# Kernel optimization log

Measured on AMD Instinct MI355X. Metric: run time of the kernel, lower is better.

Reference implementation:

```python
import jax, jax.numpy as jnp
import numpy as np

EMBED = 1024
HEADS = 16
HEAD_DIM = EMBED // HEADS


def setup_inputs() -> dict:
    key = jax.random.key(0)
    ks = jax.random.split(key, 7)
    B, Sd, Se = 4, 2048, 2048
    dec = jax.random.normal(ks[0], (B, Sd, EMBED), dtype=jnp.float32)
    enc = jax.random.normal(ks[1], (B, Se, EMBED), dtype=jnp.float32)
    scale = 1.0 / np.sqrt(EMBED)
    W_q = jax.random.normal(ks[2], (EMBED, EMBED), dtype=jnp.float32) * scale
    W_k = jax.random.normal(ks[3], (EMBED, EMBED), dtype=jnp.float32) * scale
    W_v = jax.random.normal(ks[4], (EMBED, EMBED), dtype=jnp.float32) * scale
    W_o = jax.random.normal(ks[5], (EMBED, EMBED), dtype=jnp.float32) * scale
    b_o = jax.random.normal(ks[6], (EMBED,), dtype=jnp.float32) * 0.01
    return {"decoder_input": dec, "encoder_output": enc,
            "W_q": W_q, "W_k": W_k, "W_v": W_v, "W_o": W_o, "b_o": b_o}


def reference(decoder_input, encoder_output, W_q, W_k, W_v, W_o, b_o):
    B, Sd, E = decoder_input.shape
    Se = encoder_output.shape[1]
    # projections (nn.Linear applies x @ W.T; here W is stored as [in, out])
    Q = (decoder_input @ W_q).reshape(B, Sd, HEADS, HEAD_DIM)
    K = (encoder_output @ W_k).reshape(B, Se, HEADS, HEAD_DIM)
    V = (encoder_output @ W_v).reshape(B, Se, HEADS, HEAD_DIM)
    # scores: [B, H, Sd, Se]
    scores = jnp.einsum('bqhd,bkhd->bhqk', Q, K) / jnp.sqrt(jnp.float32(HEAD_DIM))
    attn = jax.nn.softmax(scores, axis=-1)
    out = jnp.einsum('bhqk,bkhd->bqhd', attn, V).reshape(B, Sd, E)
    return out @ W_o + b_o
```

## Files before the change

kernel.cpp:

```cpp
#include <hip/hip_runtime.h>
#include <hip/hip_bf16.h>

namespace {

typedef __attribute__((ext_vector_type(8))) short bf16x8;
typedef __attribute__((ext_vector_type(4))) float f32x4;
typedef __attribute__((ext_vector_type(4))) unsigned u32x4v;

constexpr int BATCH = 4;
constexpr int SEQ   = 2048;
constexpr int EMB   = 1024;
constexpr int NH    = 16;
constexpr int HD    = 64;
constexpr int MTOT  = BATCH * SEQ;
constexpr int KVW   = 2 * EMB;
constexpr float LOG2E = 1.44269504088896f;
constexpr float SOFTMAX_C = 16.0f;

__device__ __forceinline__ unsigned short f2bf(float x) {
    unsigned int u = __float_as_uint(x);
    u += 0x7fffu + ((u >> 16) & 1u);
    return (unsigned short)(u >> 16);
}

__device__ __forceinline__ void gl_lds16(const void* g, void* l) {
    __builtin_amdgcn_global_load_lds(
        (const __attribute__((address_space(1))) unsigned int*)g,
        (__attribute__((address_space(3))) unsigned int*)l, 16, 0, 0);
}

__global__ __launch_bounds__(256)
void conv_bf16(const float* __restrict__ dec, const float* __restrict__ enc,
               unsigned short* __restrict__ decb, unsigned short* __restrict__ encb,
               int n4)
{
    int i = blockIdx.x * 256 + threadIdx.x;
    if (i >= n4) return;
    const float* src = blockIdx.y ? enc : dec;
    unsigned short* dst = blockIdx.y ? encb : decb;
    float4 v = ((const float4*)src)[i];
    ushort4 o;
    o.x = f2bf(v.x); o.y = f2bf(v.y); o.z = f2bf(v.z); o.w = f2bf(v.w);
    ((ushort4*)dst)[i] = o;
}

__global__ __launch_bounds__(256)
void wtrans(const float* __restrict__ W0, const float* __restrict__ W1,
            const float* __restrict__ W2, const float* __restrict__ W3,
            unsigned short* __restrict__ WtBase, float qscale)
{
    __shared__ __align__(16) unsigned short Ts[64][65];
    const int tid = threadIdx.x;
    const int z = blockIdx.z;
    const float* W = (z == 0) ? W0 : (z == 1) ? W1 : (z == 2) ? W2 : W3;
    unsigned short* Wt = WtBase + (size_t)z * EMB * EMB;
    const float scale = (z == 0) ? qscale : 1.0f;
    const int n0 = blockIdx.x * 64, k0 = blockIdx.y * 64;
    #pragma unroll
    for (int i = 0; i < 4; ++i) {
        int id = tid + i * 256;
        int r = id >> 4, q = id & 15;
        float4 v = *(const float4*)&W[(size_t)(k0 + r) * EMB + n0 + q * 4];
        Ts[q * 4 + 0][r] = f2bf(v.x * scale);
        Ts[q * 4 + 1][r] = f2bf(v.y * scale);
        Ts[q * 4 + 2][r] = f2bf(v.z * scale);
        Ts[q * 4 + 3][r] = f2bf(v.w * scale);
    }
    __syncthreads();
    #pragma unroll
    for (int i = 0; i < 4; ++i) {
        int id = tid + i * 256;
        int rn = id >> 4, q = id & 15;
        ushort4 o;
        o.x = Ts[rn][q * 4 + 0]; o.y = Ts[rn][q * 4 + 1];
        o.z = Ts[rn][q * 4 + 2]; o.w = Ts[rn][q * 4 + 3];
        *(ushort4*)&Wt[(size_t)(n0 + rn) * EMB + k0 + q * 4] = o;
    }
}

__global__ __launch_bounds__(256)
void vtrans(const unsigned short* __restrict__ V, unsigned short* __restrict__ Vt)
{
    __shared__ __align__(16) unsigned short Ts[64][72];
    const int tid = threadIdx.x;
    const int s0 = blockIdx.x * 64;
    const int bh = blockIdx.y, b = bh >> 4, h = bh & 15;
    #pragma unroll
    for (int it = 0; it < 2; ++it) {
        int id = tid + it * 256;
        int r = id >> 3, seg = id & 7;
        uint4 v = *(const uint4*)&V[(size_t)(b * SEQ + s0 + r) * KVW + h * HD + seg * 8];
        const unsigned short* pv = (const unsigned short*)&v;
        #pragma unroll
        for (int j = 0; j < 8; ++j) Ts[seg * 8 + j][r] = pv[j];
    }
    __syncthreads();
    #pragma unroll
    for (int it = 0; it < 2; ++it) {
        int id = tid + it * 256;
        int d = id >> 3, sg = id & 7;
        int base = (sg >> 2) * 32 + (sg & 3) * 4;
        uint2 wlo = *(const uint2*)&Ts[d][base];
        uint2 whi = *(const uint2*)&Ts[d][base + 16];
        uint4 w;
        w.x = wlo.x; w.y = wlo.y; w.z = whi.x; w.w = whi.y;
        *(uint4*)&Vt[((size_t)bh * HD + d) * SEQ + s0 + sg * 8] = w;
    }
}

template<bool OUT_BF16, bool BIAS>
__device__ __forceinline__
void gemm_body(const unsigned short* __restrict__ A, const unsigned short* __restrict__ Bt,
               const float* __restrict__ bias, void* __restrict__ Cout,
               int m0, int n0, int N, int Kd)
{
    __shared__ __align__(16) unsigned short As[2][128 * 32];
    __shared__ __align__(16) unsigned short Bs[2][128 * 32];
    const int tid  = threadIdx.x;
    const int lane = tid & 63, wave = tid >> 6;
    const int g = lane >> 4, c = lane & 15;
    const int wm = (wave & 1) * 64, wn = (wave >> 1) * 64;

    const int r0 = tid >> 2, s = tid & 3;
    const int sg = s ^ ((r0 + (r0 >> 2)) & 3);
    const unsigned short* ga0 = A  + (size_t)(m0 + r0)      * Kd + sg * 8;
    const unsigned short* ga1 = A  + (size_t)(m0 + r0 + 64) * Kd + sg * 8;
    const unsigned short* gb0 = Bt + (size_t)(n0 + r0)      * Kd + sg * 8;
    const unsigned short* gb1 = Bt + (size_t)(n0 + r0 + 64) * Kd + sg * 8;
    const int lo0 = tid * 8, lo1 = (256 + tid) * 8;

    const int cs = (c + (c >> 2)) & 3;

    f32x4 acc[4][4];
    #pragma unroll
    for (int i = 0; i < 4; ++i)
        #pragma unroll
        for (int j = 0; j < 4; ++j) acc[i][j] = (f32x4)0.0f;

    gl_lds16(ga0, &As[0][lo0]); gl_lds16(ga1, &As[0][lo1]);
    gl_lds16(gb0, &Bs[0][lo0]); gl_lds16(gb1, &Bs[0][lo1]);
    ga0 += 32; ga1 += 32; gb0 += 32; gb1 += 32;
    __syncthreads();

    const int KT = Kd / 32;
    for (int kt = 0; kt < KT; kt += 2) {
        #pragma unroll
        for (int h2 = 0; h2 < 2; ++h2) {
            const int k = kt + h2;
            if (k + 1 < KT) {
                gl_lds16(ga0, &As[h2 ^ 1][lo0]); gl_lds16(ga1, &As[h2 ^ 1][lo1]);
                gl_lds16(gb0, &Bs[h2 ^ 1][lo0]); gl_lds16(gb1, &Bs[h2 ^ 1][lo1]);
                ga0 += 32; ga1 += 32; gb0 += 32; gb1 += 32;
            }
            bf16x8 af[4], bfr[4];
            #pragma unroll
            for (int mt = 0; mt < 4; ++mt)
                af[mt]  = *(const bf16x8*)&As[h2][(wm + mt * 16 + c) * 32 + (g ^ cs) * 8];
            #pragma unroll
            for (int nt = 0; nt < 4; ++nt)
                bfr[nt] = *(const bf16x8*)&Bs[h2][(wn + nt * 16 + c) * 32 + (g ^ cs) * 8];
            #pragma unroll
            for (int mt = 0; mt < 4; ++mt)
                #pragma unroll
                for (int nt = 0; nt < 4; ++nt)
                    acc[mt][nt] = __builtin_amdgcn_mfma_f32_16x16x32_bf16(af[mt], bfr[nt], acc[mt][nt], 0, 0, 0);
            __syncthreads();
        }
    }

    #pragma unroll
    for (int mt = 0; mt < 4; ++mt) {
        #pragma unroll
        for (int nt = 0; nt < 4; ++nt) {
            int n = n0 + wn + nt * 16 + c;
            float bv = BIAS ? bias[n] : 0.0f;
            #pragma unroll
            for (int r = 0; r < 4; ++r) {
                int m = m0 + wm + mt * 16 + 4 * g + r;
                float v = acc[mt][nt][r] + bv;
                if (OUT_BF16) ((unsigned short*)Cout)[(size_t)m * N + n] = f2bf(v);
                else          ((float*)Cout)[(size_t)m * N + n] = v;
            }
        }
    }
}

__global__ __launch_bounds__(256)
void proj_fused(const unsigned short* __restrict__ decb, const unsigned short* __restrict__ encb,
                const unsigned short* __restrict__ WtBase,
                unsigned short* __restrict__ Qb, unsigned short* __restrict__ KVb)
{
    const int fid = blockIdx.y * 24 + blockIdx.x;
    const int xcd = fid & 7, idx = fid >> 3;
    const int mt  = (xcd << 3) | (idx / 24);
    const int nt  = idx % 24;
    const int m0  = mt * 128;
    if (nt < 8) {
        gemm_body<true, false>(decb, WtBase, nullptr, Qb, m0, nt * 128, EMB, EMB);
    } else {
        gemm_body<true, false>(encb, WtBase + (size_t)EMB * EMB, nullptr, KVb,
                               m0, (nt - 8) * 128, KVW, EMB);
    }
}

__global__ __launch_bounds__(256)
void proj_out(const unsigned short* __restrict__ Ob, const unsigned short* __restrict__ WoT,
              const float* __restrict__ bo, float* __restrict__ out)
{
    const int fid = blockIdx.y * 8 + blockIdx.x;
    const int xcd = fid & 7, idx = fid >> 3;
    const int mt  = (xcd << 3) | (idx >> 3);
    const int nt  = idx & 7;
    gemm_body<false, true>(Ob, WoT, bo, out, mt * 128, nt * 128, EMB, EMB);
}

__global__ __launch_bounds__(256)
void attn(const unsigned short* __restrict__ Q, const unsigned short* __restrict__ KV,
          const unsigned short* __restrict__ Vt, unsigned short* __restrict__ O)
{
    __shared__ __align__(16) unsigned short Ks[2][64 * 64];
    __shared__ __align__(16) unsigned short Vs[2][64 * 64];

    const int tid  = threadIdx.x;
    const int lane = tid & 63, wave = tid >> 6;
    const int g = lane >> 4, c = lane & 15, c7 = c & 7;

    const int fid  = blockIdx.y * 32 + blockIdx.x;
    const int xcd  = fid & 7, idx = fid >> 3;
    const int bh   = (xcd << 3) | (idx >> 5);
    const int qblk = idx & 31;
    const int b = bh >> 4, h = bh & 15;
    const int qw = qblk * 64 + wave * 16;

    const unsigned short* Qp0 = Q + (size_t)(b * SEQ + qw + c) * EMB + h * HD;
    bf16x8 qb[2];
    qb[0] = *(const bf16x8*)(Qp0 + g * 8);
    qb[1] = *(const bf16x8*)(Qp0 + 32 + g * 8);

    const int r0 = tid >> 3, s8 = tid & 7;
    const int sg = s8 ^ (r0 & 7);
    const unsigned short* gK0 = KV + ((size_t)b * SEQ + r0) * KVW + h * HD + sg * 8;
    const unsigned short* gK1 = gK0 + (size_t)32 * KVW;
    const unsigned short* gV0 = Vt + (size_t)bh * HD * SEQ + (size_t)r0 * SEQ + sg * 8;
    const unsigned short* gV1 = gV0 + (size_t)32 * SEQ;
    const int lo0 = tid * 8, lo1 = (256 + tid) * 8;

    f32x4 oac[4];
    #pragma unroll
    for (int dt = 0; dt < 4; ++dt) oac[dt] = (f32x4)0.0f;
    f32x4 lacc = (f32x4)0.0f;
    const f32x4 minit = {-SOFTMAX_C, -SOFTMAX_C, -SOFTMAX_C, -SOFTMAX_C};
    const short onebf = (short)0x3F80;
    const bf16x8 vones = {onebf, onebf, onebf, onebf, onebf, onebf, onebf, onebf};

    gl_lds16(gK0, &Ks[0][lo0]); gl_lds16(gK1, &Ks[0][lo1]);
    gl_lds16(gV0, &Vs[0][lo0]); gl_lds16(gV1, &Vs[0][lo1]);
    gK0 += (size_t)64 * KVW; gK1 += (size_t)64 * KVW; gV0 += 64; gV1 += 64;
    __syncthreads();

    constexpr int T = SEQ / 64;
    for (int t = 0; t < T; t += 2) {
        #pragma unroll
        for (int h2 = 0; h2 < 2; ++h2) {
            const int tt = t + h2;
            if (tt + 1 < T) {
                gl_lds16(gK0, &Ks[h2 ^ 1][lo0]); gl_lds16(gK1, &Ks[h2 ^ 1][lo1]);
                gl_lds16(gV0, &Vs[h2 ^ 1][lo0]); gl_lds16(gV1, &Vs[h2 ^ 1][lo1]);
                gK0 += (size_t)64 * KVW; gK1 += (size_t)64 * KVW;
                gV0 += 64;               gV1 += 64;
            }

            f32x4 st[4];
            __builtin_amdgcn_s_setprio(1);
            #pragma unroll
            for (int kt = 0; kt < 4; ++kt) {
                bf16x8 ka0 = *(const bf16x8*)&Ks[h2][(kt * 16 + c) * 64 + (g ^ c7) * 8];
                bf16x8 ka1 = *(const bf16x8*)&Ks[h2][(kt * 16 + c) * 64 + ((4 + g) ^ c7) * 8];
                st[kt] = __builtin_amdgcn_mfma_f32_16x16x32_bf16(ka0, qb[0], minit, 0, 0, 0);
                st[kt] = __builtin_amdgcn_mfma_f32_16x16x32_bf16(ka1, qb[1], st[kt], 0, 0, 0);
            }
            __builtin_amdgcn_s_setprio(0);

            bf16x8 pa[2];
            {
                unsigned uu[8];
                #pragma unroll
                for (int kt = 0; kt < 4; ++kt) {
                    float p0 = __builtin_amdgcn_exp2f(st[kt][0]);
                    float p1 = __builtin_amdgcn_exp2f(st[kt][1]);
                    float p2 = __builtin_amdgcn_exp2f(st[kt][2]);
                    float p3 = __builtin_amdgcn_exp2f(st[kt][3]);
                    asm("v_cvt_pk_bf16_f32 %0, %1, %2" : "=v"(uu[2 * kt])     : "v"(p0), "v"(p1));
                    asm("v_cvt_pk_bf16_f32 %0, %1, %2" : "=v"(uu[2 * kt + 1]) : "v"(p2), "v"(p3));
                }
                u32x4v w0 = {uu[0], uu[1], uu[2], uu[3]};
                u32x4v w1 = {uu[4], uu[5], uu[6], uu[7]};
                pa[0] = __builtin_bit_cast(bf16x8, w0);
                pa[1] = __builtin_bit_cast(bf16x8, w1);
            }

            __builtin_amdgcn_s_setprio(1);
            #pragma unroll
            for (int dt = 0; dt < 4; ++dt) {
                bf16x8 vb0 = *(const bf16x8*)&Vs[h2][(dt * 16 + c) * 64 + (g ^ c7) * 8];
                bf16x8 vb1 = *(const bf16x8*)&Vs[h2][(dt * 16 + c) * 64 + ((4 + g) ^ c7) * 8];
                oac[dt] = __builtin_amdgcn_mfma_f32_16x16x32_bf16(pa[0], vb0, oac[dt], 0, 0, 0);
                oac[dt] = __builtin_amdgcn_mfma_f32_16x16x32_bf16(pa[1], vb1, oac[dt], 0, 0, 0);
            }
            lacc = __builtin_amdgcn_mfma_f32_16x16x32_bf16(pa[0], vones, lacc, 0, 0, 0);
            lacc = __builtin_amdgcn_mfma_f32_16x16x32_bf16(pa[1], vones, lacc, 0, 0, 0);
            __builtin_amdgcn_s_setprio(0);

            __syncthreads();
        }
    }

    unsigned short* Op = O + (size_t)(b * SEQ + qw) * EMB + h * HD;
    #pragma unroll
    for (int r = 0; r < 4; ++r) {
        float linv = 1.0f / lacc[r];
        #pragma unroll
        for (int dt = 0; dt < 4; ++dt)
            Op[(size_t)(4 * g + r) * EMB + dt * 16 + c] = f2bf(oac[dt][r] * linv);
    }
}

}

extern "C" void kernel_launch(void* const* d_in, const int* in_sizes, int n_in,
                              void* d_out, int out_size, void* d_ws, size_t ws_size,
                              hipStream_t stream)
{
    const float* dec = (const float*)d_in[0];
    const float* enc = (const float*)d_in[1];
    const float* Wq  = (const float*)d_in[2];
    const float* Wk  = (const float*)d_in[3];
    const float* Wv  = (const float*)d_in[4];
    const float* Wo  = (const float*)d_in[5];
    const float* bo  = (const float*)d_in[6];
    float* out = (float*)d_out;

    const size_t BIG = (size_t)MTOT * EMB;
    const size_t SML = (size_t)EMB * EMB;
    unsigned short* decb = (unsigned short*)d_ws;
    unsigned short* encb = decb + BIG;
    unsigned short* WqT  = encb + BIG;
    unsigned short* WoT  = WqT + 3 * SML;
    unsigned short* Qb   = WqT + 4 * SML;
    unsigned short* KVb  = Qb + BIG;
    unsigned short* Vtg  = KVb + 2 * BIG;
    unsigned short* Ob   = Vtg + BIG;

    dim3 blk(256);

    conv_bf16<<<dim3((unsigned)(BIG / 4 / 256), 2), blk, 0, stream>>>(
        dec, enc, decb, encb, (int)(BIG / 4));

    wtrans<<<dim3(16, 16, 4), blk, 0, stream>>>(Wq, Wk, Wv, Wo, WqT, 0.125f * LOG2E);

    proj_fused<<<dim3(24, MTOT / 128), blk, 0, stream>>>(decb, encb, WqT, Qb, KVb);

    vtrans<<<dim3(SEQ / 64, BATCH * NH), blk, 0, stream>>>(KVb + EMB, Vtg);

    attn<<<dim3(SEQ / 64, BATCH * NH), blk, 0, stream>>>(Qb, KVb, Vtg, Ob);

    proj_out<<<dim3(EMB / 128, MTOT / 128), blk, 0, stream>>>(Ob, WoT, bo, out);
}
```

Before: 315.2 us.

## Fuse V transpose into projection epilogue and merge prep kernels

The V-projection GEMM now writes its output straight into the transposed, permuted Vt layout that the attention kernel consumes, so the separate vtrans kernel and the full V round-trip through global memory go away. K is stored in its own contiguous buffer with stride EMB instead of an interleaved KV buffer. The bf16 conversion of the activations and the weight transpose are merged into a single prep launch to save one launch and its tail. The cost is a scattered ushort4 store pattern in the V epilogue, which may coalesce less well than the old row-major stores.

Result: slower. 323.5 us (+2.6%).

```diff
diff --git a/kernel.cpp b/kernel.cpp
--- a/kernel.cpp
+++ b/kernel.cpp
@@ -13,7 +13,6 @@
 constexpr int NH    = 16;
 constexpr int HD    = 64;
 constexpr int MTOT  = BATCH * SEQ;
-constexpr int KVW   = 2 * EMB;
 constexpr float LOG2E = 1.44269504088896f;
 constexpr float SOFTMAX_C = 16.0f;
 
@@ -30,32 +29,32 @@
 }
 
 __global__ __launch_bounds__(256)
-void conv_bf16(const float* __restrict__ dec, const float* __restrict__ enc,
-               unsigned short* __restrict__ decb, unsigned short* __restrict__ encb,
-               int n4)
-{
-    int i = blockIdx.x * 256 + threadIdx.x;
-    if (i >= n4) return;
-    const float* src = blockIdx.y ? enc : dec;
-    unsigned short* dst = blockIdx.y ? encb : decb;
-    float4 v = ((const float4*)src)[i];
-    ushort4 o;
-    o.x = f2bf(v.x); o.y = f2bf(v.y); o.z = f2bf(v.z); o.w = f2bf(v.w);
-    ((ushort4*)dst)[i] = o;
-}
-
-__global__ __launch_bounds__(256)
-void wtrans(const float* __restrict__ W0, const float* __restrict__ W1,
-            const float* __restrict__ W2, const float* __restrict__ W3,
-            unsigned short* __restrict__ WtBase, float qscale)
+void prep(const float* __restrict__ dec, const float* __restrict__ enc,
+          unsigned short* __restrict__ decb, unsigned short* __restrict__ encb,
+          const float* __restrict__ W0, const float* __restrict__ W1,
+          const float* __restrict__ W2, const float* __restrict__ W3,
+          unsigned short* __restrict__ WtBase, float qscale)
 {
     __shared__ __align__(16) unsigned short Ts[64][65];
     const int tid = threadIdx.x;
-    const int z = blockIdx.z;
+    const int bid = blockIdx.x;
+    if (bid < 16384) {
+        const int zz = bid >> 13;
+        const int i = (bid & 8191) * 256 + tid;
+        const float* src = zz ? enc : dec;
+        unsigned short* dst = zz ? encb : decb;
+        float4 v = ((const float4*)src)[i];
+        ushort4 o;
+        o.x = f2bf(v.x); o.y = f2bf(v.y); o.z = f2bf(v.z); o.w = f2bf(v.w);
+        ((ushort4*)dst)[i] = o;
+        return;
+    }
+    const int zid = bid - 16384;
+    const int z = zid >> 8;
     const float* W = (z == 0) ? W0 : (z == 1) ? W1 : (z == 2) ? W2 : W3;
     unsigned short* Wt = WtBase + (size_t)z * EMB * EMB;
     const float scale = (z == 0) ? qscale : 1.0f;
-    const int n0 = blockIdx.x * 64, k0 = blockIdx.y * 64;
+    const int n0 = (zid & 15) * 64, k0 = ((zid >> 4) & 15) * 64;
     #pragma unroll
     for (int i = 0; i < 4; ++i) {
         int id = tid + i * 256;
@@ -78,37 +77,9 @@
     }
 }
 
-__global__ __launch_bounds__(256)
-void vtrans(const unsigned short* __restrict__ V, unsigned short* __restrict__ Vt)
-{
-    __shared__ __align__(16) unsigned short Ts[64][72];
-    const int tid = threadIdx.x;
-    const int s0 = blockIdx.x * 64;
-    const int bh = blockIdx.y, b = bh >> 4, h = bh & 15;
-    #pragma unroll
-    for (int it = 0; it < 2; ++it) {
-        int id = tid + it * 256;
-        int r = id >> 3, seg = id & 7;
-        uint4 v = *(const uint4*)&V[(size_t)(b * SEQ + s0 + r) * KVW + h * HD + seg * 8];
-        const unsigned short* pv = (const unsigned short*)&v;
-        #pragma unroll
-        for (int j = 0; j < 8; ++j) Ts[seg * 8 + j][r] = pv[j];
-    }
-    __syncthreads();
-    #pragma unroll
-    for (int it = 0; it < 2; ++it) {
-        int id = tid + it * 256;
-        int d = id >> 3, sg = id & 7;
-        int base = (sg >> 2) * 32 + (sg & 3) * 4;
-        uint2 wlo = *(const uint2*)&Ts[d][base];
-        uint2 whi = *(const uint2*)&Ts[d][base + 16];
-        uint4 w;
-        w.x = wlo.x; w.y = wlo.y; w.z = whi.x; w.w = whi.y;
-        *(uint4*)&Vt[((size_t)bh * HD + d) * SEQ + s0 + sg * 8] = w;
-    }
-}
-
-template<bool OUT_BF16, bool BIAS>
+enum OutKind { OUT_BF16R, OUT_F32B, OUT_VTK };
+
+template<int OK>
 __device__ __forceinline__
 void gemm_body(const unsigned short* __restrict__ A, const unsigned short* __restrict__ Bt,
                const float* __restrict__ bias, void* __restrict__ Cout,
@@ -168,18 +139,37 @@
         }
     }
 
+    if (OK == OUT_VTK) {
+        unsigned short* Vt = (unsigned short*)Cout;
+        #pragma unroll
+        for (int mt = 0; mt < 4; ++mt) {
+            int m  = m0 + wm + mt * 16 + 4 * g;
+            int bb = m >> 11, sl = m & 2047;
+            int sp = (sl & ~31) | (((sl >> 2) & 3) << 3) | (((sl >> 4) & 1) << 2);
+            #pragma unroll
+            for (int nt = 0; nt < 4; ++nt) {
+                int np = n0 + wn + nt * 16 + c - 1024;
+                ushort4 o;
+                o.x = f2bf(acc[mt][nt][0]); o.y = f2bf(acc[mt][nt][1]);
+                o.z = f2bf(acc[mt][nt][2]); o.w = f2bf(acc[mt][nt][3]);
+                *(ushort4*)&Vt[((size_t)bb * 1024 + np) * SEQ + sp] = o;
+            }
+        }
+        return;
+    }
+
     #pragma unroll
     for (int mt = 0; mt < 4; ++mt) {
         #pragma unroll
         for (int nt = 0; nt < 4; ++nt) {
             int n = n0 + wn + nt * 16 + c;
-            float bv = BIAS ? bias[n] : 0.0f;
+            float bv = (OK == OUT_F32B) ? bias[n] : 0.0f;
             #pragma unroll
             for (int r = 0; r < 4; ++r) {
                 int m = m0 + wm + mt * 16 + 4 * g + r;
                 float v = acc[mt][nt][r] + bv;
-                if (OUT_BF16) ((unsigned short*)Cout)[(size_t)m * N + n] = f2bf(v);
-                else          ((float*)Cout)[(size_t)m * N + n] = v;
+                if (OK == OUT_BF16R) ((unsigned short*)Cout)[(size_t)m * N + n] = f2bf(v);
+                else                 ((float*)Cout)[(size_t)m * N + n] = v;
             }
         }
     }
@@ -188,7 +178,8 @@
 __global__ __launch_bounds__(256)
 void proj_fused(const unsigned short* __restrict__ decb, const unsigned short* __restrict__ encb,
                 const unsigned short* __restrict__ WtBase,
-                unsigned short* __restrict__ Qb, unsigned short* __restrict__ KVb)
+                unsigned short* __restrict__ Qb, unsigned short* __restrict__ Kb,
+                unsigned short* __restrict__ Vtg)
 {
     const int fid = blockIdx.y * 24 + blockIdx.x;
     const int xcd = fid & 7, idx = fid >> 3;
@@ -196,10 +187,13 @@
     const int nt  = idx % 24;
     const int m0  = mt * 128;
     if (nt < 8) {
-        gemm_body<true, false>(decb, WtBase, nullptr, Qb, m0, nt * 128, EMB, EMB);
+        gemm_body<OUT_BF16R>(decb, WtBase, nullptr, Qb, m0, nt * 128, EMB, EMB);
+    } else if (nt < 16) {
+        gemm_body<OUT_BF16R>(encb, WtBase + (size_t)EMB * EMB, nullptr, Kb,
+                             m0, (nt - 8) * 128, EMB, EMB);
     } else {
-        gemm_body<true, false>(encb, WtBase + (size_t)EMB * EMB, nullptr, KVb,
-                               m0, (nt - 8) * 128, KVW, EMB);
+        gemm_body<OUT_VTK>(encb, WtBase + (size_t)EMB * EMB, nullptr, Vtg,
+                           m0, (nt - 8) * 128, 0, EMB);
     }
 }
 
@@ -211,11 +205,11 @@
     const int xcd = fid & 7, idx = fid >> 3;
     const int mt  = (xcd << 3) | (idx >> 3);
     const int nt  = idx & 7;
-    gemm_body<false, true>(Ob, WoT, bo, out, mt * 128, nt * 128, EMB, EMB);
+    gemm_body<OUT_F32B>(Ob, WoT, bo, out, mt * 128, nt * 128, EMB, EMB);
 }
 
 __global__ __launch_bounds__(256)
-void attn(const unsigned short* __restrict__ Q, const unsigned short* __restrict__ KV,
+void attn(const unsigned short* __restrict__ Q, const unsigned short* __restrict__ K,
           const unsigned short* __restrict__ Vt, unsigned short* __restrict__ O)
 {
     __shared__ __align__(16) unsigned short Ks[2][64 * 64];
@@ -239,8 +233,8 @@
 
     const int r0 = tid >> 3, s8 = tid & 7;
     const int sg = s8 ^ (r0 & 7);
-    const unsigned short* gK0 = KV + ((size_t)b * SEQ + r0) * KVW + h * HD + sg * 8;
-    const unsigned short* gK1 = gK0 + (size_t)32 * KVW;
+    const unsigned short* gK0 = K + ((size_t)b * SEQ + r0) * EMB + h * HD + sg * 8;
+    const unsigned short* gK1 = gK0 + (size_t)32 * EMB;
     const unsigned short* gV0 = Vt + (size_t)bh * HD * SEQ + (size_t)r0 * SEQ + sg * 8;
     const unsigned short* gV1 = gV0 + (size_t)32 * SEQ;
     const int lo0 = tid * 8, lo1 = (256 + tid) * 8;
@@ -255,7 +249,7 @@
 
     gl_lds16(gK0, &Ks[0][lo0]); gl_lds16(gK1, &Ks[0][lo1]);
     gl_lds16(gV0, &Vs[0][lo0]); gl_lds16(gV1, &Vs[0][lo1]);
-    gK0 += (size_t)64 * KVW; gK1 += (size_t)64 * KVW; gV0 += 64; gV1 += 64;
+    gK0 += (size_t)64 * EMB; gK1 += (size_t)64 * EMB; gV0 += 64; gV1 += 64;
     __syncthreads();
 
     constexpr int T = SEQ / 64;
@@ -266,7 +260,7 @@
             if (tt + 1 < T) {
                 gl_lds16(gK0, &Ks[h2 ^ 1][lo0]); gl_lds16(gK1, &Ks[h2 ^ 1][lo1]);
                 gl_lds16(gV0, &Vs[h2 ^ 1][lo0]); gl_lds16(gV1, &Vs[h2 ^ 1][lo1]);
-                gK0 += (size_t)64 * KVW; gK1 += (size_t)64 * KVW;
+                gK0 += (size_t)64 * EMB; gK1 += (size_t)64 * EMB;
                 gV0 += 64;               gV1 += 64;
             }
 
@@ -347,22 +341,18 @@
     unsigned short* WqT  = encb + BIG;
     unsigned short* WoT  = WqT + 3 * SML;
     unsigned short* Qb   = WqT + 4 * SML;
-    unsigned short* KVb  = Qb + BIG;
-    unsigned short* Vtg  = KVb + 2 * BIG;
+    unsigned short* Kb   = Qb + BIG;
+    unsigned short* Vtg  = Kb + BIG;
     unsigned short* Ob   = Vtg + BIG;
 
     dim3 blk(256);
 
-    conv_bf16<<<dim3((unsigned)(BIG / 4 / 256), 2), blk, 0, stream>>>(
-        dec, enc, decb, encb, (int)(BIG / 4));
-
-    wtrans<<<dim3(16, 16, 4), blk, 0, stream>>>(Wq, Wk, Wv, Wo, WqT, 0.125f * LOG2E);
-
-    proj_fused<<<dim3(24, MTOT / 128), blk, 0, stream>>>(decb, encb, WqT, Qb, KVb);
-
-    vtrans<<<dim3(SEQ / 64, BATCH * NH), blk, 0, stream>>>(KVb + EMB, Vtg);
-
-    attn<<<dim3(SEQ / 64, BATCH * NH), blk, 0, stream>>>(Qb, KVb, Vtg, Ob);
+    prep<<<dim3(16384 + 1024), blk, 0, stream>>>(
+        dec, enc, decb, encb, Wq, Wk, Wv, Wo, WqT, 0.125f * LOG2E);
+
+    proj_fused<<<dim3(24, MTOT / 128), blk, 0, stream>>>(decb, encb, WqT, Qb, Kb, Vtg);
+
+    attn<<<dim3(SEQ / 64, BATCH * NH), blk, 0, stream>>>(Qb, Kb, Vtg, Ob);
 
     proj_out<<<dim3(EMB / 128, MTOT / 128), blk, 0, stream>>>(Ob, WoT, bo, out);
 }
```
